# Optimization experiments

Hardware: AMD Instinct MI355X
Metric: run time of the kernel (lower is better)

## Reference

```python
import jax, jax.numpy as jnp
import numpy as np

N = 50000      # nodes
E = 600000     # edges
B = 64         # graphs in batch
DIN = 128      # input_dim
DH = 128       # hidden_dim
P = 32         # perm_length
C = 2          # num_classes
K = 2          # TAGConv hops (DGL default)


def setup_inputs() -> dict:
    key = jax.random.key(0)
    ks = jax.random.split(key, 12)
    h = jax.random.normal(ks[0], (N, DIN), dtype=jnp.float32)
    src = jax.random.randint(ks[1], (E,), 0, N, dtype=jnp.int64)
    dst = jax.random.randint(ks[2], (E,), 0, N, dtype=jnp.int64)
    graph_ids = jnp.sort(jax.random.randint(ks[3], (N,), 0, B, dtype=jnp.int64))
    perm_features = jax.random.normal(ks[4], (B, P), dtype=jnp.float32)
    s1 = 1.0 / np.sqrt((K + 1) * DIN)
    s2 = 1.0 / np.sqrt((K + 1) * DH)
    sc = 1.0 / np.sqrt(DH + P)
    W1 = jax.random.uniform(ks[5], ((K + 1) * DIN, DH), jnp.float32, -s1, s1)
    b1 = jax.random.uniform(ks[6], (DH,), jnp.float32, -s1, s1)
    W2 = jax.random.uniform(ks[7], ((K + 1) * DH, DH), jnp.float32, -s2, s2)
    b2 = jax.random.uniform(ks[8], (DH,), jnp.float32, -s2, s2)
    Wc = jax.random.uniform(ks[9], (DH + P, C), jnp.float32, -sc, sc)
    bc = jax.random.uniform(ks[10], (C,), jnp.float32, -sc, sc)
    return {"h": h, "src": src, "dst": dst, "graph_ids": graph_ids,
            "perm_features": perm_features, "W1": W1, "b1": b1,
            "W2": W2, "b2": b2, "Wc": Wc, "bc": bc}


def _tag_conv(x, src, dst, norm, W, b):
    feats = [x]
    for _ in range(K):
        m = jax.ops.segment_sum((feats[-1] * norm)[src], dst, num_segments=N)
        feats.append(m * norm)
    return jnp.concatenate(feats, axis=-1) @ W + b


def reference(h, src, dst, graph_ids, perm_features, W1, b1, W2, b2, Wc, bc):
    # symmetric norm from in-degrees, clamped at 1 (DGL convention)
    deg = jax.ops.segment_sum(jnp.ones((E,), h.dtype), dst, num_segments=N)
    norm = jnp.where(deg < 1.0, 1.0, deg)[:, None] ** -0.5  # [N,1]
    x = jax.nn.relu(_tag_conv(h, src, dst, norm, W1, b1))
    x = _tag_conv(x, src, dst, norm, W2, b2)
    # mean_nodes over batched graph
    sums = jax.ops.segment_sum(x, graph_ids, num_segments=B)          # [B,DH]
    cnt = jax.ops.segment_sum(jnp.ones((N,), x.dtype), graph_ids, num_segments=B)
    hg = sums / jnp.maximum(cnt, 1.0)[:, None]
    combined = jnp.concatenate([hg, perm_features], axis=1)           # [B,DH+P]
    return combined @ Wc + bc
```

## Files before the change

### kernel.cpp

```cpp
#include <hip/hip_runtime.h>

#define N_NODES 50000
#define N_EDGES 600000
#define B_GRAPHS 64
#define DH 128
#define PFEAT 32
#define NCLS 2
#define SCAN_BLOCKS ((N_NODES + 255) / 256)
#define NPAD (N_NODES + 128)
#define NCVT4 (N_NODES * 128 / 4)
#define WELEMS (384 * 128)

typedef __attribute__((ext_vector_type(8))) short short8v;
typedef __attribute__((ext_vector_type(4))) float float4v;
typedef __attribute__((ext_vector_type(4))) unsigned int uint4v;

__device__ __forceinline__ unsigned int f2bf(float f) {
    unsigned int u = __float_as_uint(f);
    return (u + 0x7FFFu + ((u >> 16) & 1u)) >> 16;
}
__device__ __forceinline__ float bflo(unsigned int p) { return __uint_as_float(p << 16); }
__device__ __forceinline__ float bfhi(unsigned int p) { return __uint_as_float(p & 0xFFFF0000u); }

__global__ void k_init(const float* __restrict__ W1, const float* __restrict__ W2,
                       unsigned short* __restrict__ Wt1, unsigned short* __restrict__ Wt2,
                       int* __restrict__ deg, float* __restrict__ gsum,
                       int* __restrict__ gstart,
                       unsigned short* __restrict__ h_bf, unsigned short* __restrict__ f1,
                       unsigned short* __restrict__ f2, unsigned short* __restrict__ x2) {
    int t = blockIdx.x * 256 + threadIdx.x;
    if (t < 2 * WELEMS) {
        bool second = (t >= WELEMS);
        int idx = second ? t - WELEMS : t;
        const float* W = second ? W2 : W1;
        unsigned short* Wt = second ? Wt2 : Wt1;
        int k = idx >> 7, c = idx & 127;
        Wt[c * 384 + k] = (unsigned short)f2bf(W[idx]);
    }
    if (t < N_NODES) deg[t] = 0;
    if (t < B_GRAPHS * DH) gsum[t] = 0.f;
    if (t < B_GRAPHS) gstart[t] = -1;
    if (t < 4 * 32) {
        unsigned short* bufs[4] = {h_bf, f1, f2, x2};
        uint2 z; z.x = 0u; z.y = 0u;
        ((uint2*)(bufs[t >> 5] + (size_t)N_NODES * 128))[t & 31] = z;
    }
}

__global__ void k_deg_bound(const int* __restrict__ dst, const int* __restrict__ gid,
                            int* __restrict__ deg, int* __restrict__ epos,
                            int* __restrict__ gstart) {
    int t = blockIdx.x * 256 + threadIdx.x;
    if (t < N_EDGES) {
        int pos = atomicAdd(&deg[dst[t]], 1);
        epos[t] = pos;
    }
    int n = t - N_EDGES;
    if (n >= 0 && n < N_NODES) {
        int g = gid[n];
        if (n == 0 || gid[n - 1] != g) gstart[g] = n;
    }
}

__global__ void k_norm_bsum(const int* __restrict__ deg, float* __restrict__ norm,
                            float* __restrict__ rnorm, int* __restrict__ bsum) {
    __shared__ int s[256];
    int i = blockIdx.x * 256 + threadIdx.x;
    int d = (i < N_NODES) ? deg[i] : 0;
    if (i < N_NODES) {
        int dc = d < 1 ? 1 : d;
        norm[i] = rsqrtf((float)dc);
        rnorm[i] = sqrtf((float)dc);
    }
    s[threadIdx.x] = d;
    __syncthreads();
    for (int off = 128; off > 0; off >>= 1) {
        if (threadIdx.x < off) s[threadIdx.x] += s[threadIdx.x + off];
        __syncthreads();
    }
    if (threadIdx.x == 0) bsum[blockIdx.x] = s[0];
}

__global__ void k_scan2(const int* __restrict__ deg, const int* __restrict__ bsum,
                        int* __restrict__ row_ptr) {
    __shared__ int sb[256];
    __shared__ int s[256];
    int bv = (threadIdx.x < SCAN_BLOCKS) ? bsum[threadIdx.x] : 0;
    sb[threadIdx.x] = bv;
    int i = blockIdx.x * 256 + threadIdx.x;
    int v = (i < N_NODES) ? deg[i] : 0;
    s[threadIdx.x] = v;
    __syncthreads();
    for (int off = 1; off < 256; off <<= 1) {
        int tb = (threadIdx.x >= off) ? sb[threadIdx.x - off] : 0;
        int t = (threadIdx.x >= off) ? s[threadIdx.x - off] : 0;
        __syncthreads();
        sb[threadIdx.x] += tb;
        s[threadIdx.x] += t;
        __syncthreads();
    }
    int block_off = (blockIdx.x == 0) ? 0 : sb[blockIdx.x - 1];
    if (i < N_NODES) row_ptr[i + 1] = s[threadIdx.x] + block_off;
    if (i == 0) row_ptr[0] = 0;
}

__global__ void k_scatter_cvt(const int* __restrict__ src, const int* __restrict__ dst,
                              const int* __restrict__ row_ptr, const int* __restrict__ epos,
                              int* __restrict__ col, const float* __restrict__ h,
                              const float* __restrict__ norm,
                              unsigned short* __restrict__ h_bf) {
    int t = blockIdx.x * 256 + threadIdx.x;
    if (t < N_EDGES) {
        int d = dst[t];
        col[row_ptr[d] + epos[t]] = src[t];
    }
    if (t < NCVT4) {
        float4 v = ((const float4*)h)[t];
        float nv = norm[t >> 5];
        unsigned int lo = f2bf(v.x * nv) | (f2bf(v.y * nv) << 16);
        unsigned int hi = f2bf(v.z * nv) | (f2bf(v.w * nv) << 16);
        uint2 r; r.x = lo; r.y = hi;
        ((uint2*)h_bf)[t] = r;
    }
}

__global__ __launch_bounds__(256) void k_spmm(const unsigned short* __restrict__ fin,
                                              const float* __restrict__ norm,
                                              const int* __restrict__ row_ptr,
                                              const int* __restrict__ col,
                                              unsigned short* __restrict__ fout) {
    int tid = threadIdx.x;
    int grp = tid >> 4;
    int l15 = tid & 15;
    int v = blockIdx.x * 16 + grp;
    if (v >= N_NODES) return;
    int beg = row_ptr[v], end = row_ptr[v + 1];

    float a0[8], a1[8], a2[8], a3[8];
#pragma unroll
    for (int j = 0; j < 8; ++j) { a0[j] = 0.f; a1[j] = 0.f; a2[j] = 0.f; a3[j] = 0.f; }

    int last = end - 1;
    for (int e = beg; e < end; e += 4) {
        int e1 = e + 1, e2 = e + 2, e3 = e + 3;
        int u0 = col[e];
        int u1 = col[(e1 < end) ? e1 : last];
        int u2 = col[(e2 < end) ? e2 : last];
        int u3 = col[(e3 < end) ? e3 : last];
        u1 = (e1 < end) ? u1 : N_NODES;
        u2 = (e2 < end) ? u2 : N_NODES;
        u3 = (e3 < end) ? u3 : N_NODES;
        uint4v r0 = *(const uint4v*)(fin + (size_t)u0 * 128 + l15 * 8);
        uint4v r1 = *(const uint4v*)(fin + (size_t)u1 * 128 + l15 * 8);
        uint4v r2 = *(const uint4v*)(fin + (size_t)u2 * 128 + l15 * 8);
        uint4v r3 = *(const uint4v*)(fin + (size_t)u3 * 128 + l15 * 8);
#pragma unroll
        for (int q = 0; q < 4; ++q) {
            a0[2 * q]     += bflo(r0[q]);
            a0[2 * q + 1] += bfhi(r0[q]);
            a1[2 * q]     += bflo(r1[q]);
            a1[2 * q + 1] += bfhi(r1[q]);
            a2[2 * q]     += bflo(r2[q]);
            a2[2 * q + 1] += bfhi(r2[q]);
            a3[2 * q]     += bflo(r3[q]);
            a3[2 * q + 1] += bfhi(r3[q]);
        }
    }

    float nv = norm[v];
    float s2 = nv * nv;
    uint4v o;
#pragma unroll
    for (int q = 0; q < 4; ++q) {
        float lo = (a0[2 * q] + a1[2 * q]) + (a2[2 * q] + a3[2 * q]);
        float hi = (a0[2 * q + 1] + a1[2 * q + 1]) + (a2[2 * q + 1] + a3[2 * q + 1]);
        o[q] = f2bf(lo * s2) | (f2bf(hi * s2) << 16);
    }
    *(uint4v*)(fout + (size_t)v * 128 + l15 * 8) = o;
}

template <bool RELU, bool POOL>
__global__ __launch_bounds__(256, 1) void k_gemm_mfma(const unsigned short* __restrict__ A0,
                                                      const unsigned short* __restrict__ A1,
                                                      const unsigned short* __restrict__ A2,
                                                      const unsigned short* __restrict__ Wt,
                                                      const float* __restrict__ bias,
                                                      unsigned short* __restrict__ out,
                                                      const int* __restrict__ gid,
                                                      float* __restrict__ gsum,
                                                      const float* __restrict__ normv,
                                                      const float* __restrict__ rnorm) {
    __shared__ float red4[4][128];
    int tid = threadIdx.x;
    int lane = tid & 63;
    int wid = tid >> 6;
    int l15 = lane & 15;
    int lk = lane >> 4;
    int n0 = blockIdx.x * 128;
    int rbase = n0 + wid * 32;

    float4v acc[2][8];
#pragma unroll
    for (int rt = 0; rt < 2; ++rt)
#pragma unroll
        for (int ct = 0; ct < 8; ++ct)
#pragma unroll
            for (int i = 0; i < 4; ++i) acc[rt][ct][i] = 0.f;

    const unsigned short* Aseg[3] = {A0, A1, A2};
#pragma unroll
    for (int ks = 0; ks < 12; ++ks) {
        const unsigned short* A = Aseg[ks >> 2];
        int kloc = (ks & 3) * 32 + lk * 8;
        short8v a0 = *(const short8v*)(A + (size_t)(rbase + l15) * 128 + kloc);
        short8v a1 = *(const short8v*)(A + (size_t)(rbase + 16 + l15) * 128 + kloc);
        const unsigned short* wp = Wt + (size_t)l15 * 384 + ks * 32 + lk * 8;
#pragma unroll
        for (int ct = 0; ct < 8; ++ct) {
            short8v b = *(const short8v*)(wp + (size_t)ct * 16 * 384);
            acc[0][ct] = __builtin_amdgcn_mfma_f32_16x16x32_bf16(a0, b, acc[0][ct], 0, 0, 0);
            acc[1][ct] = __builtin_amdgcn_mfma_f32_16x16x32_bf16(a1, b, acc[1][ct], 0, 0, 0);
        }
    }

    if (!POOL) {
        float bj[8];
#pragma unroll
        for (int ct = 0; ct < 8; ++ct) bj[ct] = bias[ct * 16 + l15];
#pragma unroll
        for (int rt = 0; rt < 2; ++rt)
#pragma unroll
            for (int i = 0; i < 4; ++i) {
                int row = rbase + rt * 16 + lk * 4 + i;
                if (row < N_NODES) {
                    float nv = normv[row];
#pragma unroll
                    for (int ct = 0; ct < 8; ++ct) {
                        float v = acc[rt][ct][i] + nv * bj[ct];
                        if (RELU) v = fmaxf(v, 0.f);
                        out[(size_t)row * 128 + ct * 16 + l15] = (unsigned short)f2bf(v);
                    }
                }
            }
    } else {
        int gr[2][4];
        float rn[2][4];
#pragma unroll
        for (int rt = 0; rt < 2; ++rt)
#pragma unroll
            for (int i = 0; i < 4; ++i) {
                int row = rbase + rt * 16 + lk * 4 + i;
                bool ok = (row < N_NODES);
                gr[rt][i] = ok ? gid[row] : -1;
                rn[rt][i] = ok ? rnorm[row] : 0.f;
            }
        int lastrow = n0 + 127;
        if (lastrow >= N_NODES) lastrow = N_NODES - 1;
        int gfirst = gid[n0];
        int glast = gid[lastrow];
        for (int g = gfirst; g <= glast; ++g) {
            float p[8];
#pragma unroll
            for (int ct = 0; ct < 8; ++ct) {
                float s = 0.f;
#pragma unroll
                for (int rt = 0; rt < 2; ++rt)
#pragma unroll
                    for (int i = 0; i < 4; ++i)
                        if (gr[rt][i] == g) s += rn[rt][i] * acc[rt][ct][i];
                p[ct] = s;
            }
#pragma unroll
            for (int ct = 0; ct < 8; ++ct) {
                p[ct] += __shfl_xor(p[ct], 16, 64);
                p[ct] += __shfl_xor(p[ct], 32, 64);
            }
            if (lane < 16) {
#pragma unroll
                for (int ct = 0; ct < 8; ++ct) red4[wid][ct * 16 + lane] = p[ct];
            }
            __syncthreads();
            if (tid < 128) {
                float s = red4[0][tid] + red4[1][tid] + red4[2][tid] + red4[3][tid];
                atomicAdd(&gsum[g * 128 + tid], s);
            }
            __syncthreads();
        }
    }
}

__global__ void k_final(const float* __restrict__ gsum, const int* __restrict__ gstart,
                        const float* __restrict__ b2, const float* __restrict__ perm,
                        const float* __restrict__ Wc, const float* __restrict__ bc,
                        float* __restrict__ out) {
    int t = threadIdx.x;
    if (t >= B_GRAPHS * NCLS) return;
    int b = t / NCLS, c = t % NCLS;
    int s = gstart[b];
    float cf = 1.f;
    bool nonempty = (s >= 0);
    if (nonempty) {
        int nxt = N_NODES;
        for (int j = b + 1; j < B_GRAPHS; ++j) {
            int sj = gstart[j];
            if (sj >= 0) { nxt = sj; break; }
        }
        int cnt = nxt - s;
        cf = (cnt < 1) ? 1.f : (float)cnt;
    }
    float acc = bc[c];
    for (int d = 0; d < DH; ++d) {
        float hg = gsum[b * 128 + d] / cf + (nonempty ? b2[d] : 0.f);
        acc += hg * Wc[d * NCLS + c];
    }
    for (int p = 0; p < PFEAT; ++p) acc += perm[b * PFEAT + p] * Wc[(DH + p) * NCLS + c];
    out[t] = acc;
}

extern "C" void kernel_launch(void* const* d_in, const int* in_sizes, int n_in,
                              void* d_out, int out_size, void* d_ws, size_t ws_size,
                              hipStream_t stream) {
    const float* h    = (const float*)d_in[0];
    const int*   src  = (const int*)d_in[1];
    const int*   dst  = (const int*)d_in[2];
    const int*   gid  = (const int*)d_in[3];
    const float* perm = (const float*)d_in[4];
    const float* W1   = (const float*)d_in[5];
    const float* b1   = (const float*)d_in[6];
    const float* W2   = (const float*)d_in[7];
    const float* b2   = (const float*)d_in[8];
    const float* Wc   = (const float*)d_in[9];
    const float* bc   = (const float*)d_in[10];
    float* out = (float*)d_out;

    char* ws = (char*)d_ws;
    size_t off = 0;
    auto alloc = [&](size_t bytes) {
        void* p = ws + off;
        off = (off + bytes + 255) & ~(size_t)255;
        return p;
    };
    int*   deg     = (int*)alloc(N_NODES * 4);
    int*   row_ptr = (int*)alloc((N_NODES + 1) * 4);
    int*   col     = (int*)alloc(N_EDGES * 4);
    int*   epos    = (int*)alloc(N_EDGES * 4);
    int*   bsum    = (int*)alloc(SCAN_BLOCKS * 4);
    float* norm    = (float*)alloc(N_NODES * 4);
    float* rnorm   = (float*)alloc(N_NODES * 4);
    unsigned short* h_bf = (unsigned short*)alloc((size_t)NPAD * 128 * 2);
    unsigned short* f1   = (unsigned short*)alloc((size_t)NPAD * 128 * 2);
    unsigned short* f2   = (unsigned short*)alloc((size_t)NPAD * 128 * 2);
    unsigned short* x2   = (unsigned short*)alloc((size_t)NPAD * 128 * 2);
    unsigned short* Wt1  = (unsigned short*)alloc(384 * 128 * 2);
    unsigned short* Wt2  = (unsigned short*)alloc(384 * 128 * 2);
    float* gsum    = (float*)alloc(B_GRAPHS * 128 * 4);
    int*   gstart  = (int*)alloc(B_GRAPHS * 4);

    k_init<<<(2 * WELEMS + 255) / 256, 256, 0, stream>>>(W1, W2, Wt1, Wt2,
                                                         deg, gsum, gstart,
                                                         h_bf, f1, f2, x2);
    k_deg_bound<<<(N_EDGES + N_NODES + 255) / 256, 256, 0, stream>>>(dst, gid, deg, epos, gstart);
    k_norm_bsum<<<SCAN_BLOCKS, 256, 0, stream>>>(deg, norm, rnorm, bsum);
    k_scan2<<<SCAN_BLOCKS, 256, 0, stream>>>(deg, bsum, row_ptr);
    k_scatter_cvt<<<(NCVT4 + 255) / 256, 256, 0, stream>>>(src, dst, row_ptr, epos, col,
                                                           h, norm, h_bf);

    int spmm_grid = (N_NODES + 15) / 16;
    int gemm_grid = (N_NODES + 127) / 128;

    k_spmm<<<spmm_grid, 256, 0, stream>>>(h_bf, norm, row_ptr, col, f1);
    k_spmm<<<spmm_grid, 256, 0, stream>>>(f1, norm, row_ptr, col, f2);
    k_gemm_mfma<true, false><<<gemm_grid, 256, 0, stream>>>(h_bf, f1, f2, Wt1, b1, x2,
                                                            gid, gsum, norm, rnorm);

    k_spmm<<<spmm_grid, 256, 0, stream>>>(x2, norm, row_ptr, col, f1);
    k_spmm<<<spmm_grid, 256, 0, stream>>>(f1, norm, row_ptr, col, f2);
    k_gemm_mfma<false, true><<<gemm_grid, 256, 0, stream>>>(x2, f1, f2, Wt2, nullptr, nullptr,
                                                            gid, gsum, norm, rnorm);

    k_final<<<1, 128, 0, stream>>>(gsum, gstart, b2, perm, Wc, bc, out);
}
```

Baseline: 227.1 us.

## Split K dimension across two wave groups in MFMA GEMM blocks

The GEMM block grows from 4 to 8 waves. Each group of four waves computes half of the 12 K-steps for the same 128-row tile, and the two partial accumulators are combined through a 64 KB shared-memory buffer before the epilogue. The pooling reduction is widened to 8 waves, with the zeroed second-half accumulators contributing nothing. The aim is more waves per CU to hide load and MFMA latency on a grid that barely fills the device. The cost is a large LDS footprint, an extra barrier and an LDS round-trip of the whole accumulator tile.

```diff
diff --git a/kernel.cpp b/kernel.cpp
--- a/kernel.cpp
+++ b/kernel.cpp
@@ -180,7 +180,7 @@
 }
 
 template <bool RELU, bool POOL>
-__global__ __launch_bounds__(256, 1) void k_gemm_mfma(const unsigned short* __restrict__ A0,
+__global__ __launch_bounds__(512, 1) void k_gemm_mfma(const unsigned short* __restrict__ A0,
                                                       const unsigned short* __restrict__ A1,
                                                       const unsigned short* __restrict__ A2,
                                                       const unsigned short* __restrict__ Wt,
@@ -190,14 +190,17 @@
                                                       float* __restrict__ gsum,
                                                       const float* __restrict__ normv,
                                                       const float* __restrict__ rnorm) {
-    __shared__ float red4[4][128];
+    __shared__ float comb[4][64 * 64];
+    __shared__ float red8[8][128];
     int tid = threadIdx.x;
     int lane = tid & 63;
     int wid = tid >> 6;
+    int rg = wid & 3;
+    int khalf = wid >> 2;
     int l15 = lane & 15;
     int lk = lane >> 4;
     int n0 = blockIdx.x * 128;
-    int rbase = n0 + wid * 32;
+    int rbase = n0 + rg * 32;
 
     float4v acc[2][8];
 #pragma unroll
@@ -209,7 +212,8 @@
 
     const unsigned short* Aseg[3] = {A0, A1, A2};
 #pragma unroll
-    for (int ks = 0; ks < 12; ++ks) {
+    for (int s = 0; s < 6; ++s) {
+        int ks = khalf * 6 + s;
         const unsigned short* A = Aseg[ks >> 2];
         int kloc = (ks & 3) * 32 + lk * 8;
         short8v a0 = *(const short8v*)(A + (size_t)(rbase + l15) * 128 + kloc);
@@ -223,25 +227,52 @@
         }
     }
 
+    if (khalf == 1) {
+#pragma unroll
+        for (int rt = 0; rt < 2; ++rt)
+#pragma unroll
+            for (int ct = 0; ct < 8; ++ct)
+#pragma unroll
+                for (int i = 0; i < 4; ++i) {
+                    int idx = rt * 32 + ct * 4 + i;
+                    comb[rg][idx * 64 + lane] = acc[rt][ct][i];
+                    acc[rt][ct][i] = 0.f;
+                }
+    }
+    __syncthreads();
+    if (khalf == 0) {
+#pragma unroll
+        for (int rt = 0; rt < 2; ++rt)
+#pragma unroll
+            for (int ct = 0; ct < 8; ++ct)
+#pragma unroll
+                for (int i = 0; i < 4; ++i) {
+                    int idx = rt * 32 + ct * 4 + i;
+                    acc[rt][ct][i] += comb[rg][idx * 64 + lane];
+                }
+    }
+
     if (!POOL) {
-        float bj[8];
-#pragma unroll
-        for (int ct = 0; ct < 8; ++ct) bj[ct] = bias[ct * 16 + l15];
-#pragma unroll
-        for (int rt = 0; rt < 2; ++rt)
-#pragma unroll
-            for (int i = 0; i < 4; ++i) {
-                int row = rbase + rt * 16 + lk * 4 + i;
-                if (row < N_NODES) {
-                    float nv = normv[row];
-#pragma unroll
-                    for (int ct = 0; ct < 8; ++ct) {
-                        float v = acc[rt][ct][i] + nv * bj[ct];
-                        if (RELU) v = fmaxf(v, 0.f);
-                        out[(size_t)row * 128 + ct * 16 + l15] = (unsigned short)f2bf(v);
+        if (khalf == 0) {
+            float bj[8];
+#pragma unroll
+            for (int ct = 0; ct < 8; ++ct) bj[ct] = bias[ct * 16 + l15];
+#pragma unroll
+            for (int rt = 0; rt < 2; ++rt)
+#pragma unroll
+                for (int i = 0; i < 4; ++i) {
+                    int row = rbase + rt * 16 + lk * 4 + i;
+                    if (row < N_NODES) {
+                        float nv = normv[row];
+#pragma unroll
+                        for (int ct = 0; ct < 8; ++ct) {
+                            float v = acc[rt][ct][i] + nv * bj[ct];
+                            if (RELU) v = fmaxf(v, 0.f);
+                            out[(size_t)row * 128 + ct * 16 + l15] = (unsigned short)f2bf(v);
+                        }
                     }
                 }
-            }
+        }
     } else {
         int gr[2][4];
         float rn[2][4];
@@ -277,11 +308,13 @@
             }
             if (lane < 16) {
 #pragma unroll
-                for (int ct = 0; ct < 8; ++ct) red4[wid][ct * 16 + lane] = p[ct];
+                for (int ct = 0; ct < 8; ++ct) red8[wid][ct * 16 + lane] = p[ct];
             }
             __syncthreads();
             if (tid < 128) {
-                float s = red4[0][tid] + red4[1][tid] + red4[2][tid] + red4[3][tid];
+                float s = 0.f;
+#pragma unroll
+                for (int w = 0; w < 8; ++w) s += red8[w][tid];
                 atomicAdd(&gsum[g * 128 + tid], s);
             }
             __syncthreads();
@@ -370,12 +403,12 @@
 
     k_spmm<<<spmm_grid, 256, 0, stream>>>(h_bf, norm, row_ptr, col, f1);
     k_spmm<<<spmm_grid, 256, 0, stream>>>(f1, norm, row_ptr, col, f2);
-    k_gemm_mfma<true, false><<<gemm_grid, 256, 0, stream>>>(h_bf, f1, f2, Wt1, b1, x2,
+    k_gemm_mfma<true, false><<<gemm_grid, 512, 0, stream>>>(h_bf, f1, f2, Wt1, b1, x2,
                                                             gid, gsum, norm, rnorm);
 
     k_spmm<<<spmm_grid, 256, 0, stream>>>(x2, norm, row_ptr, col, f1);
     k_spmm<<<spmm_grid, 256, 0, stream>>>(f1, norm, row_ptr, col, f2);
-    k_gemm_mfma<false, true><<<gemm_grid, 256, 0, stream>>>(x2, f1, f2, Wt2, nullptr, nullptr,
+    k_gemm_mfma<false, true><<<gemm_grid, 512, 0, stream>>>(x2, f1, f2, Wt2, nullptr, nullptr,
                                                             gid, gsum, norm, rnorm);
 
     k_final<<<1, 128, 0, stream>>>(gsum, gstart, b2, perm, Wc, bc, out);
```

Result: no change. 226.8 us (-0.1%).
